# Kernel tuning notes

Hardware: AMD Instinct MI355X
Metric: run time of the kernel (lower is better)

## Reference

```python
import jax, jax.numpy as jnp
import numpy as np

N_NODES = 100000
N_EDGES = 3200000
N_GRAPHS = 2048


def setup_inputs() -> dict:
    key = jax.random.key(0)
    ks = jax.random.split(key, 6)
    x = jax.random.normal(ks[0], (N_NODES, 5), dtype=jnp.float32)
    edge_index = jax.random.randint(ks[1], (2, N_EDGES), 0, N_NODES, dtype=jnp.int64)
    batch = jnp.sort(jax.random.randint(ks[2], (N_NODES,), 0, N_GRAPHS, dtype=jnp.int64))
    # Glorot-ish init for GCN weights
    W1 = jax.random.normal(ks[3], (5, 30), dtype=jnp.float32) * (1.0 / np.sqrt(5.0))
    b1 = jnp.zeros((30,), dtype=jnp.float32)
    W2 = jax.random.normal(ks[4], (30, 8), dtype=jnp.float32) * (1.0 / np.sqrt(30.0))
    b2 = jnp.zeros((8,), dtype=jnp.float32)
    return {"x": x, "edge_index": edge_index, "batch": batch,
            "W1": W1, "b1": b1, "W2": W2, "b2": b2}


def _gcn_conv(x, src, dst, W, b, n_nodes):
    # PyG GCNConv: linear transform, then D^-1/2 A_hat D^-1/2 aggregation (self-loops included in src/dst).
    h = x @ W                                              # [N, out]
    deg = jax.ops.segment_sum(jnp.ones_like(dst, dtype=h.dtype), dst, num_segments=n_nodes)
    dinv = jnp.where(deg > 0, deg ** -0.5, 0.0)            # [N]
    norm = dinv[src] * dinv[dst]                           # [E+N]
    msg = h[src] * norm[:, None]                           # gather + scale
    out = jax.ops.segment_sum(msg, dst, num_segments=n_nodes)  # scatter-add
    return out + b


def reference(x, edge_index, batch, W1, b1, W2, b2):
    n = x.shape[0]
    loops = jnp.arange(n, dtype=edge_index.dtype)
    src = jnp.concatenate([edge_index[0], loops])          # add self-loops
    dst = jnp.concatenate([edge_index[1], loops])

    h = _gcn_conv(x, src, dst, W1, b1, n)
    h = jax.nn.relu(h)
    # F.dropout with training=False (eval mode) is identity
    h = _gcn_conv(h, src, dst, W2, b2, n)                   # [N, 8]

    # scatter_mean over graph ids
    sums = jax.ops.segment_sum(h, batch, num_segments=N_GRAPHS)          # [G, 8]
    counts = jax.ops.segment_sum(jnp.ones((n,), dtype=h.dtype), batch, num_segments=N_GRAPHS)
    return sums / jnp.maximum(counts, 1.0)[:, None]
```

## Files before the change

kernel.cpp:

```cpp
#include <hip/hip_runtime.h>

#define N_NODES 100000
#define N_EDGES 3200000
#define N_GRAPHS 2048
#define SSH 8
#define SSZ 256
#define NSB 391
#define FILL_BLOCKS 512
#define CHUNK 6250
#define CAP 9216

__device__ __forceinline__ void gAtomAdd(float* p, float v) { unsafeAtomicAdd(p, v); }

__global__ void kAB_fill(const int* __restrict__ src, const int* __restrict__ dst,
                         int* __restrict__ bcnt, unsigned* __restrict__ stage) {
  __shared__ int hist[NSB];
  int tid = threadIdx.x, blk = blockIdx.x;
  for (int i = tid; i < NSB; i += 256) hist[i] = 0;
  __syncthreads();
  int beg = blk * CHUNK, end = beg + CHUNK;
  for (int e = beg + tid; e < end; e += 256) atomicAdd(&hist[dst[e] >> SSH], 1);
  __syncthreads();
  for (int i = tid; i < NSB; i += 256) {
    int h = hist[i];
    if (h) hist[i] = atomicAdd(&bcnt[i], h);
  }
  __syncthreads();
  for (int e = beg + tid; e < end; e += 256) {
    int d = dst[e], s = src[e];
    int b = d >> SSH;
    int pos = atomicAdd(&hist[b], 1);
    stage[(size_t)b * CAP + pos] = ((unsigned)s << SSH) | (unsigned)(d & (SSZ - 1));
  }
}

__global__ void k_bscan(const int* __restrict__ bcnt, int* __restrict__ sboffs) {
  __shared__ int sh[512];
  int tid = threadIdx.x;
  int v = (tid < NSB) ? bcnt[tid] : 0;
  sh[tid] = v;
  __syncthreads();
  for (int off = 1; off < 512; off <<= 1) {
    int t = (tid >= off) ? sh[tid - off] : 0;
    __syncthreads();
    sh[tid] += t;
    __syncthreads();
  }
  if (tid < NSB) sboffs[tid] = sh[tid] - v;
  if (tid == 0) sboffs[NSB] = N_EDGES;
}

__global__ void kC_csr(const unsigned* __restrict__ stage, const int* __restrict__ bcnt,
                       const int* __restrict__ sboffs, const float* __restrict__ x,
                       int* __restrict__ noffs, float* __restrict__ dinv,
                       float* __restrict__ xd8, int* __restrict__ csr) {
  __shared__ int cnt[SSZ], sc[SSZ], cur[SSZ];
  int b = blockIdx.x, tid = threadIdx.x;
  cnt[tid] = 0;
  __syncthreads();
  size_t rbeg = (size_t)b * CAP;
  int n_in_b = bcnt[b];
  int wbeg = sboffs[b];
  for (int k = tid; k < n_in_b; k += 256) atomicAdd(&cnt[stage[rbeg + k] & (SSZ - 1)], 1);
  __syncthreads();
  sc[tid] = cnt[tid];
  __syncthreads();
  for (int off = 1; off < SSZ; off <<= 1) {
    int t = (tid >= off) ? sc[tid - off] : 0;
    __syncthreads();
    sc[tid] += t;
    __syncthreads();
  }
  int excl = sc[tid] - cnt[tid];
  int node = b * SSZ + tid;
  if (node <= N_NODES) noffs[node] = wbeg + excl;
  if (node < N_NODES) {
    float di = rsqrtf((float)(cnt[tid] + 1));
    dinv[node] = di;
    float r[5];
#pragma unroll
    for (int c = 0; c < 5; c++) r[c] = x[node * 5 + c] * di;
    float4* xv = (float4*)xd8;
    xv[node * 2]     = make_float4(r[0], r[1], r[2], r[3]);
    xv[node * 2 + 1] = make_float4(r[4], 0.f, 0.f, 0.f);
  }
  cur[tid] = wbeg + excl;
  __syncthreads();
  for (int k = tid; k < n_in_b; k += 256) {
    unsigned u = stage[rbeg + k];
    int pos = atomicAdd(&cur[u & (SSZ - 1)], 1);
    csr[pos] = (int)(u >> SSH);
  }
}

__global__ void k_agg1(const int* __restrict__ csr, const int* __restrict__ noffs,
                       const float* __restrict__ xd8, const float* __restrict__ dinv,
                       const float* __restrict__ W1, const float* __restrict__ b1,
                       const float* __restrict__ W2, float* __restrict__ g2) {
  __shared__ float w1[150], bb1[30], w2[240];
  int tid = threadIdx.x;
  for (int i = tid; i < 150; i += 256) w1[i] = W1[i];
  for (int i = tid; i < 30; i += 256) bb1[i] = b1[i];
  for (int i = tid; i < 240; i += 256) w2[i] = W2[i];
  __syncthreads();
  int n = blockIdx.x * 256 + tid;
  if (n >= N_NODES) return;
  const float4* xv = (const float4*)xd8;
  float a0 = 0, a1 = 0, a2 = 0, a3 = 0, a4 = 0;
  int k = noffs[n], end = noffs[n + 1];
  for (; k + 4 <= end; k += 4) {
    int s0 = csr[k], s1 = csr[k + 1], s2 = csr[k + 2], s3 = csr[k + 3];
    float4 q0 = xv[s0 * 2], q1 = xv[s1 * 2], q2 = xv[s2 * 2], q3 = xv[s3 * 2];
    float c0 = xd8[s0 * 8 + 4], c1 = xd8[s1 * 8 + 4], c2 = xd8[s2 * 8 + 4], c3 = xd8[s3 * 8 + 4];
    a0 += q0.x + q1.x + q2.x + q3.x;
    a1 += q0.y + q1.y + q2.y + q3.y;
    a2 += q0.z + q1.z + q2.z + q3.z;
    a3 += q0.w + q1.w + q2.w + q3.w;
    a4 += c0 + c1 + c2 + c3;
  }
  for (; k < end; k++) {
    int s = csr[k];
    float4 q = xv[s * 2];
    a0 += q.x; a1 += q.y; a2 += q.z; a3 += q.w; a4 += xd8[s * 8 + 4];
  }
  float di = dinv[n];
  float t[5] = {(a0 + xd8[n * 8 + 0]) * di, (a1 + xd8[n * 8 + 1]) * di,
                (a2 + xd8[n * 8 + 2]) * di, (a3 + xd8[n * 8 + 3]) * di,
                (a4 + xd8[n * 8 + 4]) * di};
  float h[30];
#pragma unroll
  for (int j = 0; j < 30; j++) h[j] = bb1[j];
#pragma unroll
  for (int kk = 0; kk < 5; kk++)
#pragma unroll
    for (int j = 0; j < 30; j++) h[j] += t[kk] * w1[kk * 30 + j];
  float g[8] = {0, 0, 0, 0, 0, 0, 0, 0};
#pragma unroll
  for (int j = 0; j < 30; j++) {
    float hj = fmaxf(h[j], 0.f);
#pragma unroll
    for (int c = 0; c < 8; c++) g[c] += hj * w2[j * 8 + c];
  }
  float4* gv = (float4*)g2;
  gv[n * 2]     = make_float4(g[0] * di, g[1] * di, g[2] * di, g[3] * di);
  gv[n * 2 + 1] = make_float4(g[4] * di, g[5] * di, g[6] * di, g[7] * di);
}

__global__ void k_agg2(const int* __restrict__ csr, const int* __restrict__ noffs,
                       const float* __restrict__ g2, const float* __restrict__ dinv,
                       const float* __restrict__ b2, const int* __restrict__ batch,
                       float* __restrict__ gsum) {
  __shared__ float gpool[64 * 8];
  __shared__ float bb2[8];
  __shared__ int batch0s;
  int blk = blockIdx.x, tid = threadIdx.x;
  for (int i = tid; i < 64 * 8; i += 256) gpool[i] = 0.f;
  if (tid < 8) bb2[tid] = b2[tid];
  if (tid == 0) {
    int n0 = blk * 256;
    batch0s = batch[n0 < N_NODES ? n0 : (N_NODES - 1)];
  }
  __syncthreads();
  int n = blk * 256 + tid;
  int batch0 = batch0s;
  if (n < N_NODES) {
    const float4* gv = (const float4*)g2;
    float4 lo = make_float4(0, 0, 0, 0), hi = make_float4(0, 0, 0, 0);
    int k = noffs[n], end = noffs[n + 1];
    for (; k + 2 <= end; k += 2) {
      int s0 = csr[k], s1 = csr[k + 1];
      float4 p0 = gv[s0 * 2], q0 = gv[s0 * 2 + 1];
      float4 p1 = gv[s1 * 2], q1 = gv[s1 * 2 + 1];
      lo.x += p0.x + p1.x; lo.y += p0.y + p1.y;
      lo.z += p0.z + p1.z; lo.w += p0.w + p1.w;
      hi.x += q0.x + q1.x; hi.y += q0.y + q1.y;
      hi.z += q0.z + q1.z; hi.w += q0.w + q1.w;
    }
    for (; k < end; k++) {
      int s = csr[k];
      float4 p = gv[s * 2], q = gv[s * 2 + 1];
      lo.x += p.x; lo.y += p.y; lo.z += p.z; lo.w += p.w;
      hi.x += q.x; hi.y += q.y; hi.z += q.z; hi.w += q.w;
    }
    float di = dinv[n];
    float4 sl = gv[n * 2], sh = gv[n * 2 + 1];
    float val[8] = {di * (lo.x + sl.x) + bb2[0], di * (lo.y + sl.y) + bb2[1],
                    di * (lo.z + sl.z) + bb2[2], di * (lo.w + sl.w) + bb2[3],
                    di * (hi.x + sh.x) + bb2[4], di * (hi.y + sh.y) + bb2[5],
                    di * (hi.z + sh.z) + bb2[6], di * (hi.w + sh.w) + bb2[7]};
    int gid = batch[n], goff = gid - batch0;
#pragma unroll
    for (int c = 0; c < 8; c++) {
      if (goff < 64) atomicAdd(&gpool[goff * 8 + c], val[c]);
      else           gAtomAdd(&gsum[gid * 8 + c], val[c]);
    }
  }
  __syncthreads();
  for (int i = tid; i < 64 * 8; i += 256) {
    int gid = batch0 + (i >> 3);
    float v = gpool[i];
    if (gid < N_GRAPHS && v != 0.f) gAtomAdd(&gsum[gid * 8 + (i & 7)], v);
  }
}

__global__ void k_final(const float* __restrict__ gsum, const int* __restrict__ batch,
                        float* __restrict__ out) {
  int i = blockIdx.x * 256 + threadIdx.x;
  if (i >= N_GRAPHS * 8) return;
  int g = i >> 3;
  int lo = 0, hi = N_NODES;
  while (lo < hi) { int m = (lo + hi) >> 1; if (batch[m] < g) lo = m + 1; else hi = m; }
  int lo2 = lo, hi2 = N_NODES;
  while (lo2 < hi2) { int m = (lo2 + hi2) >> 1; if (batch[m] <= g) lo2 = m + 1; else hi2 = m; }
  float c = (float)(lo2 - lo);
  out[i] = gsum[i] / fmaxf(c, 1.f);
}

extern "C" void kernel_launch(void* const* d_in, const int* in_sizes, int n_in,
                              void* d_out, int out_size, void* d_ws, size_t ws_size,
                              hipStream_t stream) {
  const float* x    = (const float*)d_in[0];
  const int* ei     = (const int*)d_in[1];
  const int* batch  = (const int*)d_in[2];
  const float* W1   = (const float*)d_in[3];
  const float* b1   = (const float*)d_in[4];
  const float* W2   = (const float*)d_in[5];
  const float* b2   = (const float*)d_in[6];
  const int* srcp = ei;
  const int* dstp = ei + N_EDGES;
  float* out = (float*)d_out;

  char* base = (char*)d_ws;
  size_t o = 0;
  auto carve = [&](size_t bytes) -> char* {
    char* p = base + o;
    o += (bytes + 255) & ~(size_t)255;
    return p;
  };
  int* bcnt        = (int*)carve((size_t)NSB * 4);
  int* sboffs      = (int*)carve((size_t)(NSB + 1) * 4);
  unsigned* stage  = (unsigned*)carve((size_t)NSB * CAP * 4);
  int* csr         = (int*)carve((size_t)N_EDGES * 4);
  int* noffs       = (int*)carve((size_t)(N_NODES + 2) * 4);
  float* dinv      = (float*)carve((size_t)N_NODES * 4);
  float* xd8       = (float*)carve((size_t)N_NODES * 8 * 4);
  float* g2        = (float*)carve((size_t)N_NODES * 8 * 4);
  float* gsum      = (float*)carve((size_t)N_GRAPHS * 8 * 4);

  hipMemsetAsync(bcnt, 0, (size_t)NSB * 4, stream);
  hipMemsetAsync(gsum, 0, (size_t)N_GRAPHS * 8 * 4, stream);

  kAB_fill<<<FILL_BLOCKS, 256, 0, stream>>>(srcp, dstp, bcnt, stage);
  k_bscan<<<1, 512, 0, stream>>>(bcnt, sboffs);
  kC_csr<<<NSB, 256, 0, stream>>>(stage, bcnt, sboffs, x, noffs, dinv, xd8, csr);
  k_agg1<<<(N_NODES + 255) / 256, 256, 0, stream>>>(csr, noffs, xd8, dinv, W1, b1, W2, g2);
  k_agg2<<<(N_NODES + 255) / 256, 256, 0, stream>>>(csr, noffs, g2, dinv, b2, batch, gsum);
  k_final<<<64, 256, 0, stream>>>(gsum, batch, out);
}
```

Measured before the change: 191.4 us.

## Write-combine bucket staging through shared memory with padded 64-byte flushes

Replaces the scattered per-edge global stores in the bucketing pass with per-bucket shared-memory buffers. Each bucket is flushed to the staging array in full 16-element (64-byte) groups, and partial tails are padded with sentinel values. Each bucket region is reserved in padded increments, which adds a second counter array, and the CSR build pass now skips sentinels. This targets write amplification from uncoalesced 4-byte scatters, at the cost of fewer, larger blocks, serialized per-bucket flush loops, and extra padding traffic.

```diff
diff --git a/kernel.cpp b/kernel.cpp
--- a/kernel.cpp
+++ b/kernel.cpp
@@ -6,38 +6,82 @@
 #define SSH 8
 #define SSZ 256
 #define NSB 391
-#define FILL_BLOCKS 512
-#define CHUNK 6250
-#define CAP 9216
+#define CAP 12800
+#define WC_BLOCKS 256
+#define WC_THREADS 1024
+#define WC_EPB 12500
+#define WC_SUB 4096
+#define CAPB 56
+#define SENT 0xFFFFFFFFu
 
 __device__ __forceinline__ void gAtomAdd(float* p, float v) { unsafeAtomicAdd(p, v); }
 
-__global__ void kAB_fill(const int* __restrict__ src, const int* __restrict__ dst,
-                         int* __restrict__ bcnt, unsigned* __restrict__ stage) {
-  __shared__ int hist[NSB];
+__global__ void kAB_wc(const int* __restrict__ src, const int* __restrict__ dst,
+                       int* __restrict__ bpad, int* __restrict__ rcnt,
+                       unsigned* __restrict__ stage) {
+  __shared__ int lbase[NSB], ctr[NSB];
+  extern __shared__ unsigned buf[];
   int tid = threadIdx.x, blk = blockIdx.x;
-  for (int i = tid; i < NSB; i += 256) hist[i] = 0;
-  __syncthreads();
-  int beg = blk * CHUNK, end = beg + CHUNK;
-  for (int e = beg + tid; e < end; e += 256) atomicAdd(&hist[dst[e] >> SSH], 1);
-  __syncthreads();
-  for (int i = tid; i < NSB; i += 256) {
-    int h = hist[i];
-    if (h) hist[i] = atomicAdd(&bcnt[i], h);
-  }
-  __syncthreads();
-  for (int e = beg + tid; e < end; e += 256) {
-    int d = dst[e], s = src[e];
-    int b = d >> SSH;
-    int pos = atomicAdd(&hist[b], 1);
-    stage[(size_t)b * CAP + pos] = ((unsigned)s << SSH) | (unsigned)(d & (SSZ - 1));
-  }
-}
-
-__global__ void k_bscan(const int* __restrict__ bcnt, int* __restrict__ sboffs) {
+  int beg = blk * WC_EPB, end = beg + WC_EPB;
+  for (int i = tid; i < NSB; i += WC_THREADS) ctr[i] = 0;
+  __syncthreads();
+  for (int e = beg + tid; e < end; e += WC_THREADS)
+    atomicAdd(&ctr[dst[e] >> SSH], 1);
+  __syncthreads();
+  for (int i = tid; i < NSB; i += WC_THREADS) {
+    int h = ctr[i];
+    int hp = (h + 15) & ~15;
+    int base = 0;
+    if (hp) base = atomicAdd(&bpad[i], hp);
+    if (h) atomicAdd(&rcnt[i], h);
+    lbase[i] = i * CAP + base;
+    ctr[i] = 0;
+  }
+  __syncthreads();
+  for (int sc = 0; sc < WC_EPB; sc += WC_SUB) {
+    int send = beg + sc + WC_SUB; if (send > end) send = end;
+    for (int e = beg + sc + tid; e < send; e += WC_THREADS) {
+      int d = dst[e], s = src[e];
+      int b = d >> SSH;
+      int pos = atomicAdd(&ctr[b], 1);
+      buf[b * CAPB + pos] = ((unsigned)s << SSH) | (unsigned)(d & (SSZ - 1));
+    }
+    __syncthreads();
+    for (int b = tid; b < NSB; b += WC_THREADS) {
+      int c = ctr[b];
+      int g = c >> 4;
+      if (g) {
+        unsigned* bb = &buf[b * CAPB];
+        int gb = lbase[b];
+        for (int q = 0; q < g; q++) {
+          uint4* dp = (uint4*)&stage[gb + q * 16];
+          const uint4* sp = (const uint4*)&bb[q * 16];
+          dp[0] = sp[0]; dp[1] = sp[1]; dp[2] = sp[2]; dp[3] = sp[3];
+        }
+        lbase[b] = gb + g * 16;
+        int rem = c & 15;
+        for (int j = 0; j < rem; j++) bb[j] = bb[g * 16 + j];
+        ctr[b] = rem;
+      }
+    }
+    __syncthreads();
+  }
+  for (int b = tid; b < NSB; b += WC_THREADS) {
+    int c = ctr[b];
+    if (c) {
+      unsigned* bb = &buf[b * CAPB];
+      for (int j = c; j < 16; j++) bb[j] = SENT;
+      uint4* dp = (uint4*)&stage[lbase[b]];
+      const uint4* sp = (const uint4*)bb;
+      dp[0] = sp[0]; dp[1] = sp[1]; dp[2] = sp[2]; dp[3] = sp[3];
+    }
+  }
+}
+
+__global__ void k_bscan(const int* __restrict__ rcnt, int* __restrict__ sboffs) {
   __shared__ int sh[512];
   int tid = threadIdx.x;
-  int v = (tid < NSB) ? bcnt[tid] : 0;
+  int v = (tid < NSB) ? rcnt[tid] : 0;
   sh[tid] = v;
   __syncthreads();
   for (int off = 1; off < 512; off <<= 1) {
@@ -50,7 +94,7 @@
   if (tid == 0) sboffs[NSB] = N_EDGES;
 }
 
-__global__ void kC_csr(const unsigned* __restrict__ stage, const int* __restrict__ bcnt,
+__global__ void kC_csr(const unsigned* __restrict__ stage, const int* __restrict__ bpad,
                        const int* __restrict__ sboffs, const float* __restrict__ x,
                        int* __restrict__ noffs, float* __restrict__ dinv,
                        float* __restrict__ xd8, int* __restrict__ csr) {
@@ -59,9 +103,12 @@
   cnt[tid] = 0;
   __syncthreads();
   size_t rbeg = (size_t)b * CAP;
-  int n_in_b = bcnt[b];
+  int pcnt = bpad[b];
   int wbeg = sboffs[b];
-  for (int k = tid; k < n_in_b; k += 256) atomicAdd(&cnt[stage[rbeg + k] & (SSZ - 1)], 1);
+  for (int k = tid; k < pcnt; k += 256) {
+    unsigned u = stage[rbeg + k];
+    if (u != SENT) atomicAdd(&cnt[u & (SSZ - 1)], 1);
+  }
   __syncthreads();
   sc[tid] = cnt[tid];
   __syncthreads();
@@ -86,10 +133,12 @@
   }
   cur[tid] = wbeg + excl;
   __syncthreads();
-  for (int k = tid; k < n_in_b; k += 256) {
+  for (int k = tid; k < pcnt; k += 256) {
     unsigned u = stage[rbeg + k];
-    int pos = atomicAdd(&cur[u & (SSZ - 1)], 1);
-    csr[pos] = (int)(u >> SSH);
+    if (u != SENT) {
+      int pos = atomicAdd(&cur[u & (SSZ - 1)], 1);
+      csr[pos] = (int)(u >> SSH);
+    }
   }
 }
 
@@ -237,7 +286,8 @@
     o += (bytes + 255) & ~(size_t)255;
     return p;
   };
-  int* bcnt        = (int*)carve((size_t)NSB * 4);
+  int* bpad        = (int*)carve((size_t)NSB * 4);
+  int* rcnt        = (int*)carve((size_t)NSB * 4);
   int* sboffs      = (int*)carve((size_t)(NSB + 1) * 4);
   unsigned* stage  = (unsigned*)carve((size_t)NSB * CAP * 4);
   int* csr         = (int*)carve((size_t)N_EDGES * 4);
@@ -247,12 +297,17 @@
   float* g2        = (float*)carve((size_t)N_NODES * 8 * 4);
   float* gsum      = (float*)carve((size_t)N_GRAPHS * 8 * 4);
 
-  hipMemsetAsync(bcnt, 0, (size_t)NSB * 4, stream);
+  (void)hipFuncSetAttribute(reinterpret_cast<const void*>(&kAB_wc),
+                            hipFuncAttributeMaxDynamicSharedMemorySize,
+                            NSB * CAPB * 4);
+
+  hipMemsetAsync(bpad, 0, (size_t)NSB * 4, stream);
+  hipMemsetAsync(rcnt, 0, (size_t)NSB * 4, stream);
   hipMemsetAsync(gsum, 0, (size_t)N_GRAPHS * 8 * 4, stream);
 
-  kAB_fill<<<FILL_BLOCKS, 256, 0, stream>>>(srcp, dstp, bcnt, stage);
-  k_bscan<<<1, 512, 0, stream>>>(bcnt, sboffs);
-  kC_csr<<<NSB, 256, 0, stream>>>(stage, bcnt, sboffs, x, noffs, dinv, xd8, csr);
+  kAB_wc<<<WC_BLOCKS, WC_THREADS, NSB * CAPB * 4, stream>>>(srcp, dstp, bpad, rcnt, stage);
+  k_bscan<<<1, 512, 0, stream>>>(rcnt, sboffs);
+  kC_csr<<<NSB, 256, 0, stream>>>(stage, bpad, sboffs, x, noffs, dinv, xd8, csr);
   k_agg1<<<(N_NODES + 255) / 256, 256, 0, stream>>>(csr, noffs, xd8, dinv, W1, b1, W2, g2);
   k_agg2<<<(N_NODES + 255) / 256, 256, 0, stream>>>(csr, noffs, g2, dinv, b2, batch, gsum);
   k_final<<<64, 256, 0, stream>>>(gsum, batch, out);
```

Result: faster. 184.8 us, median of 2 (-3.4%).
